# Kernel tuning notes

Hardware: AMD Instinct MI355X
Metric: run time of the kernel (lower is better)

Reference implementation:

```python
import jax, jax.numpy as jnp
import numpy as np

N_NODES = 100000
N_EDGES = 1600000
EMBED_DIM = 64


def setup_inputs() -> dict:
    key = jax.random.key(0)
    k_x, k_e, k_w, k_b = jax.random.split(key, 4)
    x = jax.random.normal(k_x, (N_NODES, EMBED_DIM), dtype=jnp.float32)
    edge_index = jax.random.randint(k_e, (2, N_EDGES), 0, N_NODES, dtype=jnp.int64)
    # nn.Linear(embed_dim, embed_dim): weight [out, in], bias [out]
    W = jax.random.normal(k_w, (EMBED_DIM, EMBED_DIM), dtype=jnp.float32) * (1.0 / np.sqrt(EMBED_DIM))
    b = jax.random.normal(k_b, (EMBED_DIM,), dtype=jnp.float32) * 0.01
    return {"x": x, "edge_index": edge_index, "W": W, "b": b, "num_node": N_NODES}


def reference(x, edge_index, W, b, num_node):
    source_nodes, target_nodes = edge_index[0], edge_index[1]
    # h = relu(Linear(x))  -> [N, d]
    h = jax.nn.relu(jnp.einsum("nd,od->no", x, W) + b)
    # gather messages at target nodes: [E, d]
    msgs = h[target_nodes]
    # scatter-add into source node slots (index_add_)
    aggr = jax.ops.segment_sum(msgs, source_nodes, num_segments=num_node)
    # mean normalization: bincount clamped to >= 1
    counts = jnp.bincount(source_nodes, length=num_node).astype(jnp.float32)
    counts = jnp.maximum(counts, 1.0)
    # dropout is identity at inference (training=False)
    return aggr / counts[:, None]
```

## Files before the change

kernel.cpp:

```cpp
#include <hip/hip_runtime.h>
#include <hip/hip_bf16.h>

#define DIM 64
#define SCAN_B 256

__global__ void detect_layout_kernel(const int* __restrict__ ei32,
                                     int* __restrict__ flag) {
  int v = ei32[2 * threadIdx.x + 1];
  unsigned long long m = __ballot(v != 0);
  if (threadIdx.x == 0) *flag = (m == 0ULL) ? 1 : 0;
}

__device__ __forceinline__ int load_idx(const int* ei32, int is64, size_t pos) {
  return is64 ? ei32[2 * pos] : ei32[pos];
}

__global__ __launch_bounds__(256) void lin_hist_kernel(
    const float* __restrict__ x, const float* __restrict__ W,
    const float* __restrict__ b, float* __restrict__ h, int N, int nbLin,
    const int* __restrict__ ei32, const int* __restrict__ flag,
    int* __restrict__ counts, int* __restrict__ rank, int E) {
  __shared__ float Ws[DIM * DIM];
  __shared__ float bs[DIM];

  if (blockIdx.x >= nbLin) {
    int e = (blockIdx.x - nbLin) * 256 + threadIdx.x;
    if (e < E) {
      int src = load_idx(ei32, *flag, (size_t)e);
      int r = atomicAdd(&counts[src], 1);
      __builtin_nontemporal_store(r, &rank[e]);
    }
    return;
  }

  for (int i = threadIdx.x; i < DIM * DIM; i += 256) Ws[i] = W[i];
  if (threadIdx.x < DIM) bs[threadIdx.x] = b[threadIdx.x];
  __syncthreads();

  int row = blockIdx.x * 256 + threadIdx.x;
  if (row >= N) return;

  const float4* xr = (const float4*)(x + (size_t)row * DIM);
  float acc[DIM];
#pragma unroll
  for (int o = 0; o < DIM; ++o) acc[o] = bs[o];

#pragma unroll
  for (int i4 = 0; i4 < DIM / 4; ++i4) {
    float4 xv = xr[i4];
#pragma unroll
    for (int o = 0; o < DIM; ++o) {
      const float* wrow = &Ws[o * DIM + i4 * 4];
      acc[o] = fmaf(xv.x, wrow[0], acc[o]);
      acc[o] = fmaf(xv.y, wrow[1], acc[o]);
      acc[o] = fmaf(xv.z, wrow[2], acc[o]);
      acc[o] = fmaf(xv.w, wrow[3], acc[o]);
    }
  }

  float4* hr = (float4*)(h + (size_t)row * DIM);
#pragma unroll
  for (int o4 = 0; o4 < DIM / 4; ++o4) {
    float4 v;
    v.x = fmaxf(acc[o4 * 4 + 0], 0.0f);
    v.y = fmaxf(acc[o4 * 4 + 1], 0.0f);
    v.z = fmaxf(acc[o4 * 4 + 2], 0.0f);
    v.w = fmaxf(acc[o4 * 4 + 3], 0.0f);
    hr[o4] = v;
  }
}

__global__ void scan1_kernel(const int* __restrict__ counts,
                             int* __restrict__ offsets,
                             int* __restrict__ partials, int N) {
  __shared__ int s[SCAN_B];
  int t = threadIdx.x;
  int i = blockIdx.x * SCAN_B + t;
  int v = (i < N) ? counts[i] : 0;
  s[t] = v;
  __syncthreads();
  for (int off = 1; off < SCAN_B; off <<= 1) {
    int add = (t >= off) ? s[t - off] : 0;
    __syncthreads();
    s[t] += add;
    __syncthreads();
  }
  if (i < N) offsets[i] = s[t] - v;
  if (t == SCAN_B - 1) partials[blockIdx.x] = s[t];
}

__global__ void scan2_kernel(int* __restrict__ partials, int nb) {
  __shared__ int s[512];
  int t = threadIdx.x;
  int v = (t < nb) ? partials[t] : 0;
  s[t] = v;
  __syncthreads();
  for (int off = 1; off < 512; off <<= 1) {
    int add = (t >= off) ? s[t - off] : 0;
    __syncthreads();
    s[t] += add;
    __syncthreads();
  }
  if (t < nb) partials[t] = s[t] - v;
}

__global__ void scan3_kernel(int* __restrict__ offsets,
                             const int* __restrict__ partials, int N) {
  int i = blockIdx.x * SCAN_B + threadIdx.x;
  if (i < N) offsets[i] += partials[blockIdx.x];
}

__global__ __launch_bounds__(256) void place_kernel(
    const int* __restrict__ ei32, const int* __restrict__ flag,
    const int* __restrict__ offsets, const int* __restrict__ rank,
    int* __restrict__ bucket, int E) {
  int e = blockIdx.x * 256 + threadIdx.x;
  if (e >= E) return;
  int is64 = *flag;
  int src = load_idx(ei32, is64, (size_t)e);
  int tgt = load_idx(ei32, is64, (size_t)E + e);
  int r = __builtin_nontemporal_load(&rank[e]);
  __builtin_nontemporal_store(tgt, &bucket[offsets[src] + r]);
}

__global__ __launch_bounds__(256) void gather_kernel(
    const float* __restrict__ h, const int* __restrict__ offsets,
    const int* __restrict__ counts, const int* __restrict__ bucket,
    float* __restrict__ out, int N) {
  int wid = (blockIdx.x * 256 + threadIdx.x) >> 6;
  int lane = threadIdx.x & 63;
  if (wid >= N) return;

  int deg = counts[wid];
  int start = offsets[wid];
  float a0 = 0.f, a1 = 0.f, a2 = 0.f, a3 = 0.f;
  float a4 = 0.f, a5 = 0.f, a6 = 0.f, a7 = 0.f;

  for (int j0 = 0; j0 < deg; j0 += 64) {
    int m = min(deg - j0, 64);
    int t = (lane < m) ? __builtin_nontemporal_load(&bucket[start + j0 + lane])
                       : 0;
    int j = 0;
    for (; j + 8 <= m; j += 8) {
      int t0 = __shfl(t, j);
      int t1 = __shfl(t, j + 1);
      int t2 = __shfl(t, j + 2);
      int t3 = __shfl(t, j + 3);
      int t4 = __shfl(t, j + 4);
      int t5 = __shfl(t, j + 5);
      int t6 = __shfl(t, j + 6);
      int t7 = __shfl(t, j + 7);
      float v0 = h[(size_t)t0 * DIM + lane];
      float v1 = h[(size_t)t1 * DIM + lane];
      float v2 = h[(size_t)t2 * DIM + lane];
      float v3 = h[(size_t)t3 * DIM + lane];
      float v4 = h[(size_t)t4 * DIM + lane];
      float v5 = h[(size_t)t5 * DIM + lane];
      float v6 = h[(size_t)t6 * DIM + lane];
      float v7 = h[(size_t)t7 * DIM + lane];
      a0 += v0; a1 += v1; a2 += v2; a3 += v3;
      a4 += v4; a5 += v5; a6 += v6; a7 += v7;
    }
    for (; j < m; ++j) {
      int tj = __shfl(t, j);
      a0 += h[(size_t)tj * DIM + lane];
    }
  }

  float c = (float)max(deg, 1);
  float acc = ((a0 + a1) + (a2 + a3)) + ((a4 + a5) + (a6 + a7));
  __builtin_nontemporal_store(acc / c, &out[(size_t)wid * DIM + lane]);
}

extern "C" void kernel_launch(void* const* d_in, const int* in_sizes, int n_in,
                              void* d_out, int out_size, void* d_ws, size_t ws_size,
                              hipStream_t stream) {
  const float* x = (const float*)d_in[0];
  const int* ei32 = (const int*)d_in[1];
  const float* W = (const float*)d_in[2];
  const float* b = (const float*)d_in[3];

  const int N = in_sizes[0] / DIM;
  const int E = in_sizes[1] / 2;

  float* out = (float*)d_out;

  int* rank = (int*)d_out;

  char* p = (char*)d_ws;
  int* bucket = (int*)p;   p += (size_t)E * 4;
  int* counts = (int*)p;   p += (size_t)N * 4;
  int* offsets = (int*)p;  p += (size_t)N * 4;
  int* partials = (int*)p; p += 512 * 4;
  int* flag = (int*)p;     p += 16;
  p = (char*)(((uintptr_t)p + 15) & ~(uintptr_t)15);
  float* h = (float*)p;

  const int nb1 = (N + SCAN_B - 1) / SCAN_B;
  const int eb = (E + 255) / 256;
  const int nbLin = (N + 255) / 256;

  hipMemsetAsync(counts, 0, (size_t)N * 4, stream);

  detect_layout_kernel<<<1, 64, 0, stream>>>(ei32, flag);

  lin_hist_kernel<<<nbLin + eb, 256, 0, stream>>>(x, W, b, h, N, nbLin, ei32,
                                                  flag, counts, rank, E);

  scan1_kernel<<<nb1, SCAN_B, 0, stream>>>(counts, offsets, partials, N);
  scan2_kernel<<<1, 512, 0, stream>>>(partials, nb1);
  scan3_kernel<<<nb1, SCAN_B, 0, stream>>>(offsets, partials, N);

  place_kernel<<<eb, 256, 0, stream>>>(ei32, flag, offsets, rank, bucket, E);

  gather_kernel<<<(N * 64 + 255) / 256, 256, 0, stream>>>(h, offsets, counts,
                                                          bucket, out, N);
}
```

Measured before the change: 308.2 us.

## Privatize degree histogram per XCD with workgroup-scope atomics

After: 321.6 us. 1.04x slower.

```diff
diff --git a/kernel.cpp b/kernel.cpp
--- a/kernel.cpp
+++ b/kernel.cpp
@@ -3,6 +3,7 @@
 
 #define DIM 64
 #define SCAN_B 256
+#define NXCD 8
 
 __global__ void detect_layout_kernel(const int* __restrict__ ei32,
                                      int* __restrict__ flag) {
@@ -15,24 +16,11 @@
   return is64 ? ei32[2 * pos] : ei32[pos];
 }
 
-__global__ __launch_bounds__(256) void lin_hist_kernel(
+__global__ __launch_bounds__(256) void linear_relu_kernel(
     const float* __restrict__ x, const float* __restrict__ W,
-    const float* __restrict__ b, float* __restrict__ h, int N, int nbLin,
-    const int* __restrict__ ei32, const int* __restrict__ flag,
-    int* __restrict__ counts, int* __restrict__ rank, int E) {
+    const float* __restrict__ b, float* __restrict__ h, int N) {
   __shared__ float Ws[DIM * DIM];
   __shared__ float bs[DIM];
-
-  if (blockIdx.x >= nbLin) {
-    int e = (blockIdx.x - nbLin) * 256 + threadIdx.x;
-    if (e < E) {
-      int src = load_idx(ei32, *flag, (size_t)e);
-      int r = atomicAdd(&counts[src], 1);
-      __builtin_nontemporal_store(r, &rank[e]);
-    }
-    return;
-  }
-
   for (int i = threadIdx.x; i < DIM * DIM; i += 256) Ws[i] = W[i];
   if (threadIdx.x < DIM) bs[threadIdx.x] = b[threadIdx.x];
   __syncthreads();
@@ -70,14 +58,44 @@
   }
 }
 
-__global__ void scan1_kernel(const int* __restrict__ counts,
+__global__ __launch_bounds__(256) void hist_xcd_kernel(
+    const int* __restrict__ ei32, const int* __restrict__ flag,
+    int* __restrict__ counts8, int* __restrict__ rank,
+    int* __restrict__ chunk_xcd, int N, int E) {
+  unsigned int xcc;
+  asm volatile("s_getreg_b32 %0, hwreg(HW_REG_XCC_ID)" : "=s"(xcc));
+  xcc &= (NXCD - 1);
+  if (threadIdx.x == 0) chunk_xcd[blockIdx.x] = (int)xcc;
+
+  int e = blockIdx.x * 256 + threadIdx.x;
+  if (e >= E) return;
+  int src = load_idx(ei32, *flag, (size_t)e);
+  int* ctr = counts8 + (size_t)xcc * N + src;
+  int r = __hip_atomic_fetch_add(ctr, 1, __ATOMIC_RELAXED,
+                                 __HIP_MEMORY_SCOPE_WORKGROUP);
+  __builtin_nontemporal_store(r, &rank[e]);
+}
+
+__global__ void scan1_kernel(int* __restrict__ counts8, int* __restrict__ ctot,
                              int* __restrict__ offsets,
                              int* __restrict__ partials, int N) {
   __shared__ int s[SCAN_B];
   int t = threadIdx.x;
   int i = blockIdx.x * SCAN_B + t;
-  int v = (i < N) ? counts[i] : 0;
-  s[t] = v;
+  int total = 0;
+  if (i < N) {
+    int run = 0;
+#pragma unroll
+    for (int x = 0; x < NXCD; ++x) {
+      size_t idx = (size_t)x * N + i;
+      int c = counts8[idx];
+      counts8[idx] = run;
+      run += c;
+    }
+    total = run;
+    ctot[i] = total;
+  }
+  s[t] = total;
   __syncthreads();
   for (int off = 1; off < SCAN_B; off <<= 1) {
     int add = (t >= off) ? s[t - off] : 0;
@@ -85,7 +103,7 @@
     s[t] += add;
     __syncthreads();
   }
-  if (i < N) offsets[i] = s[t] - v;
+  if (i < N) offsets[i] = s[t] - total;
   if (t == SCAN_B - 1) partials[blockIdx.x] = s[t];
 }
 
@@ -112,26 +130,29 @@
 
 __global__ __launch_bounds__(256) void place_kernel(
     const int* __restrict__ ei32, const int* __restrict__ flag,
-    const int* __restrict__ offsets, const int* __restrict__ rank,
-    int* __restrict__ bucket, int E) {
+    const int* __restrict__ offsets, const int* __restrict__ counts8,
+    const int* __restrict__ rank, const int* __restrict__ chunk_xcd,
+    int* __restrict__ bucket, int N, int E) {
   int e = blockIdx.x * 256 + threadIdx.x;
   if (e >= E) return;
   int is64 = *flag;
+  int xcd = chunk_xcd[blockIdx.x];
   int src = load_idx(ei32, is64, (size_t)e);
   int tgt = load_idx(ei32, is64, (size_t)E + e);
   int r = __builtin_nontemporal_load(&rank[e]);
-  __builtin_nontemporal_store(tgt, &bucket[offsets[src] + r]);
+  int pos = offsets[src] + counts8[(size_t)xcd * N + src] + r;
+  bucket[pos] = tgt;
 }
 
 __global__ __launch_bounds__(256) void gather_kernel(
     const float* __restrict__ h, const int* __restrict__ offsets,
-    const int* __restrict__ counts, const int* __restrict__ bucket,
+    const int* __restrict__ ctot, const int* __restrict__ bucket,
     float* __restrict__ out, int N) {
   int wid = (blockIdx.x * 256 + threadIdx.x) >> 6;
   int lane = threadIdx.x & 63;
   if (wid >= N) return;
 
-  int deg = counts[wid];
+  int deg = ctot[wid];
   int start = offsets[wid];
   float a0 = 0.f, a1 = 0.f, a2 = 0.f, a3 = 0.f;
   float a4 = 0.f, a5 = 0.f, a6 = 0.f, a7 = 0.f;
@@ -184,35 +205,38 @@
   const int E = in_sizes[1] / 2;
 
   float* out = (float*)d_out;
-
   int* rank = (int*)d_out;
 
+  const int eb = (E + 255) / 256;
   char* p = (char*)d_ws;
-  int* bucket = (int*)p;   p += (size_t)E * 4;
-  int* counts = (int*)p;   p += (size_t)N * 4;
-  int* offsets = (int*)p;  p += (size_t)N * 4;
-  int* partials = (int*)p; p += 512 * 4;
-  int* flag = (int*)p;     p += 16;
+  int* bucket = (int*)p;    p += (size_t)E * 4;
+  int* counts8 = (int*)p;   p += (size_t)NXCD * N * 4;
+  int* ctot = (int*)p;      p += (size_t)N * 4;
+  int* offsets = (int*)p;   p += (size_t)N * 4;
+  int* partials = (int*)p;  p += 512 * 4;
+  int* flag = (int*)p;      p += 16;
+  int* chunk_xcd = (int*)p; p += (size_t)eb * 4;
   p = (char*)(((uintptr_t)p + 15) & ~(uintptr_t)15);
   float* h = (float*)p;
 
   const int nb1 = (N + SCAN_B - 1) / SCAN_B;
-  const int eb = (E + 255) / 256;
-  const int nbLin = (N + 255) / 256;
-
-  hipMemsetAsync(counts, 0, (size_t)N * 4, stream);
+
+  hipMemsetAsync(counts8, 0, (size_t)NXCD * N * 4, stream);
 
   detect_layout_kernel<<<1, 64, 0, stream>>>(ei32, flag);
 
-  lin_hist_kernel<<<nbLin + eb, 256, 0, stream>>>(x, W, b, h, N, nbLin, ei32,
-                                                  flag, counts, rank, E);
-
-  scan1_kernel<<<nb1, SCAN_B, 0, stream>>>(counts, offsets, partials, N);
+  linear_relu_kernel<<<(N + 255) / 256, 256, 0, stream>>>(x, W, b, h, N);
+
+  hist_xcd_kernel<<<eb, 256, 0, stream>>>(ei32, flag, counts8, rank,
+                                          chunk_xcd, N, E);
+
+  scan1_kernel<<<nb1, SCAN_B, 0, stream>>>(counts8, ctot, offsets, partials, N);
   scan2_kernel<<<1, 512, 0, stream>>>(partials, nb1);
   scan3_kernel<<<nb1, SCAN_B, 0, stream>>>(offsets, partials, N);
 
-  place_kernel<<<eb, 256, 0, stream>>>(ei32, flag, offsets, rank, bucket, E);
-
-  gather_kernel<<<(N * 64 + 255) / 256, 256, 0, stream>>>(h, offsets, counts,
+  place_kernel<<<eb, 256, 0, stream>>>(ei32, flag, offsets, counts8, rank,
+                                       chunk_xcd, bucket, N, E);
+
+  gather_kernel<<<(N * 64 + 255) / 256, 256, 0, stream>>>(h, offsets, ctot,
                                                           bucket, out, N);
 }
```
